# Performance work log

Measured on AMD Instinct MI355X. Metric: run time of the kernel, lower is better.

## Reference

```python
import jax, jax.numpy as jnp
import numpy as np


def setup_inputs() -> dict:
    key = jax.random.key(0)
    k1, k2, k3 = jax.random.split(key, 3)
    B, c_in, T, N = 16, 64, 64, 512
    K, c_out = 3, 64
    x = jax.random.normal(k1, (B, c_in, T, N), dtype=jnp.float32)
    # scaled Laplacian-like matrix; scale to keep Chebyshev recurrence stable
    La = jax.random.normal(k2, (B, N, N), dtype=jnp.float32) / jnp.sqrt(jnp.float32(N))
    # Conv2d(K*c_in, c_out, 1x1, bias=False) weight, squeezed to [c_out, K*c_in]
    W = jax.random.normal(k3, (c_out, K * c_in), dtype=jnp.float32) * 0.05
    return {"x": x, "La": La, "W": W}


def reference(x, La, W):
    # x: [B, c_in, T, N], La: [B, N, N], W: [c_out, K*c_in]
    B, c_in, T, N = x.shape
    K = W.shape[1] // c_in
    xp = jnp.transpose(x, (0, 1, 3, 2))  # [B, c_in, N, T] -> 'bcnl'
    # Chebyshev polynomial recurrence: T0 = I, T1 = La, Tk = 2*La@T_{k-1} - T_{k-2}
    I = jnp.broadcast_to(jnp.eye(N, dtype=x.dtype), (B, N, N))
    Ls = [I, La]
    L0, L1 = I, La
    for _ in range(2, K):
        L2 = 2.0 * jnp.matmul(La, L1) - L0
        L0, L1 = L1, L2
        Ls.append(L2)
    Lap = jnp.stack(Ls, axis=1)            # [B, K, N, N]
    Lap = jnp.swapaxes(Lap, -1, -2)        # transpose(-1,-2) as in torch
    # graph conv: contract over source node n
    y = jnp.einsum('bcnl,bknq->bckql', xp, Lap)  # [B, c_in, K, N, T]
    y = y.reshape(B, c_in * K, N, T)       # channel index = c*K + k
    # 1x1 conv, no bias: [c_out, c_in*K] x [B, c_in*K, N, T]
    out = jnp.einsum('oi,binl->bonl', W, y)  # [B, c_out, N, T]
    out = jnp.transpose(out, (0, 1, 3, 2))   # [B, c_out, T, N]
    return out
```

## Files before the change

### kernel.cpp

```cpp
#include <hip/hip_runtime.h>
#include <hip/hip_bf16.h>


#define B_   16
#define CIN  64
#define T_   64
#define N_   512
#define M_   4096
#define KDIM 512
#define COUT 64

typedef __bf16 bf16x8 __attribute__((ext_vector_type(8)));
typedef float  floatx4 __attribute__((ext_vector_type(4)));

__device__ __forceinline__ float bf2f(unsigned short u) {
    unsigned int v = ((unsigned int)u) << 16;
    return __builtin_bit_cast(float, v);
}
__device__ __forceinline__ unsigned short f2bf(float f) {
    unsigned int u = __builtin_bit_cast(unsigned int, f);
    unsigned int lsb = (u >> 16) & 1u;
    u += 0x7fffu + lsb;
    return (unsigned short)(u >> 16);
}

#define GLOAD_LDS16(gp, lp)                                                  \
    __builtin_amdgcn_global_load_lds(                                        \
        (const __attribute__((address_space(1))) void*)(gp),                 \
        (__attribute__((address_space(3))) void*)(lp), 16, 0, 0)

__global__ __launch_bounds__(256) void cvt_f32_bf16(
    const float* __restrict__ src, unsigned short* __restrict__ dst, int n)
{
    int i = (blockIdx.x * 256 + threadIdx.x) * 8;
    if (i + 8 <= n) {
        float4 a = *(const float4*)(src + i);
        float4 b = *(const float4*)(src + i + 4);
        union { unsigned short s[8]; uint4 u; } o;
        o.s[0] = f2bf(a.x); o.s[1] = f2bf(a.y); o.s[2] = f2bf(a.z); o.s[3] = f2bf(a.w);
        o.s[4] = f2bf(b.x); o.s[5] = f2bf(b.y); o.s[6] = f2bf(b.z); o.s[7] = f2bf(b.w);
        *(uint4*)(dst + i) = o.u;
    }
}

__global__ __launch_bounds__(256) void pack_w(
    const float* __restrict__ W, unsigned short* __restrict__ Wb)
{
    int idx = threadIdx.x + blockIdx.x * 256;
    if (idx < 64 * 192) {
        int o = idx / 192, j = idx % 192;
        int c = j & 63, k = j >> 6;
        Wb[idx] = f2bf(W[o * 192 + c * 3 + k]);
    }
}

#define BM 128
#define BN 128
#define BK 32
#define KIT  (KDIM / BK)
#define SBUF (BM * BK)

__global__ __launch_bounds__(256) void gemm_bt(
    const unsigned short* __restrict__ A,
    const unsigned short* __restrict__ Bm,
    unsigned short* __restrict__ C,
    const unsigned short* __restrict__ X,
    int mode)
{
    int h     = blockIdx.x;
    int g     = h & 7;
    int idx   = h >> 3;
    int batch = g * 2 + (idx >> 7);
    int local = idx & 127;
    int n0    = (local & 3) * BN;
    int m0    = (local >> 2) * BM;

    A  += (size_t)batch * M_ * KDIM;
    Bm += (size_t)batch * N_ * KDIM;
    C  += (size_t)batch * M_ * N_;
    X  += (size_t)batch * M_ * N_;

    __shared__ __align__(16) unsigned short As[3 * SBUF];
    __shared__ __align__(16) unsigned short Bs[3 * SBUF];

    int tid  = threadIdx.x;
    int lane = tid & 63;
    int wave = tid >> 6;
    int wm   = (wave >> 1) * 64;
    int wn   = (wave & 1) * 64;
    int l15  = lane & 15;
    int quad = lane >> 4;

    int r16 = lane >> 2;
    int sch = lane & 3;
    int gch = sch ^ ((r16 >> 1) & 3);

    const unsigned short* gA0 = A  + (size_t)(m0 + wave * 16 + r16) * KDIM + gch * 8;
    const unsigned short* gA1 = gA0 + (size_t)64 * KDIM;
    const unsigned short* gB0 = Bm + (size_t)(n0 + wave * 16 + r16) * KDIM + gch * 8;
    const unsigned short* gB1 = gB0 + (size_t)64 * KDIM;

    int dA0 = (wave * 16) * BK;
    int dA1 = (64 + wave * 16) * BK;
    int dB0 = dA0;
    int dB1 = dA1;

#define STAGE(kk, bo) do {                                        \
        GLOAD_LDS16(gA0 + (kk) * BK, &As[(bo) + dA0]);            \
        GLOAD_LDS16(gA1 + (kk) * BK, &As[(bo) + dA1]);            \
        GLOAD_LDS16(gB0 + (kk) * BK, &Bs[(bo) + dB0]);            \
        GLOAD_LDS16(gB1 + (kk) * BK, &Bs[(bo) + dB1]);            \
    } while (0)

    int aoff[4], boff[4];
    int sl = quad ^ ((l15 >> 1) & 3);
#pragma unroll
    for (int im = 0; im < 4; im++)
        aoff[im] = (wm + im * 16 + l15) * BK + sl * 8;
#pragma unroll
    for (int jn = 0; jn < 4; jn++)
        boff[jn] = (wn + jn * 16 + l15) * BK + sl * 8;

    floatx4 acc[4][4];
#pragma unroll
    for (int i = 0; i < 4; i++)
#pragma unroll
        for (int j = 0; j < 4; j++) acc[i][j] = (floatx4)0.0f;

    STAGE(0, 0);
    STAGE(1, SBUF);

#pragma unroll
    for (int k = 0; k < KIT; ++k) {
        if (k < KIT - 1) asm volatile("s_waitcnt vmcnt(4)" ::: "memory");
        else             asm volatile("s_waitcnt vmcnt(0)" ::: "memory");
        __builtin_amdgcn_s_barrier();

        if (k + 2 < KIT) STAGE(k + 2, ((k + 2) % 3) * SBUF);

        const int cb = (k % 3) * SBUF;
        bf16x8 af[4], bf[4];
#pragma unroll
        for (int im = 0; im < 4; im++)
            af[im] = __builtin_bit_cast(bf16x8, *(const uint4*)&As[cb + aoff[im]]);
#pragma unroll
        for (int jn = 0; jn < 4; jn++)
            bf[jn] = __builtin_bit_cast(bf16x8, *(const uint4*)&Bs[cb + boff[jn]]);
#pragma unroll
        for (int im = 0; im < 4; im++)
#pragma unroll
            for (int jn = 0; jn < 4; jn++)
                acc[im][jn] = __builtin_amdgcn_mfma_f32_16x16x32_bf16(
                    af[im], bf[jn], acc[im][jn], 0, 0, 0);
    }
#undef STAGE

#pragma unroll
    for (int im = 0; im < 4; im++)
#pragma unroll
        for (int jn = 0; jn < 4; jn++) {
            int c = n0 + wn + jn * 16 + l15;
#pragma unroll
            for (int r = 0; r < 4; r++) {
                int m = m0 + wm + im * 16 + quad * 4 + r;
                size_t idx2 = (size_t)m * N_ + c;
                float v = acc[im][jn][r];
                if (mode) v = 2.0f * v - bf2f(X[idx2]);
                C[idx2] = f2bf(v);
            }
        }
}

#define PJ_PITCH 40

__global__ __launch_bounds__(256) void proj(
    const unsigned short* __restrict__ xb,
    const unsigned short* __restrict__ z1b,
    const unsigned short* __restrict__ z2b,
    const unsigned short* __restrict__ Wb,
    float* __restrict__ out)
{
    __shared__ __align__(16) unsigned short Ds[256 * PJ_PITCH];

    int b  = blockIdx.y;
    int n0 = blockIdx.x * 256;
    int tid  = threadIdx.x;
    int lane = tid & 63;
    int wave = tid >> 6;
    int l15  = lane & 15;
    int quad = lane >> 4;

    size_t boff = (size_t)b * M_ * N_ + n0;
    const unsigned short* zp[3] = { xb + boff, z1b + boff, z2b + boff };

    bf16x8 wf[6];
#pragma unroll
    for (int kc = 0; kc < 6; kc++)
        wf[kc] = __builtin_bit_cast(bf16x8,
            *(const uint4*)(Wb + (size_t)(wave * 16 + l15) * 192 + kc * 32 + quad * 8));

    floatx4 acc[16];
#pragma unroll
    for (int i = 0; i < 16; i++) acc[i] = (floatx4)0.0f;

    int jl  = tid & 31;
    int nc0 = (tid >> 5) * 8;

    for (int kc = 0; kc < 6; kc++) {
        const unsigned short* src =
            zp[kc >> 1] + (size_t)((kc & 1) * 32 + jl) * (T_ * N_) + nc0;
        uint4 v[4];
#pragma unroll
        for (int u = 0; u < 4; u++) v[u] = *(const uint4*)(src + u * 64);

        __syncthreads();
#pragma unroll
        for (int u = 0; u < 4; u++) {
            unsigned short* d = &Ds[(size_t)(nc0 + u * 64) * PJ_PITCH + jl];
            unsigned int w0 = v[u].x, w1 = v[u].y, w2 = v[u].z, w3 = v[u].w;
            d[0 * PJ_PITCH] = (unsigned short)w0;
            d[1 * PJ_PITCH] = (unsigned short)(w0 >> 16);
            d[2 * PJ_PITCH] = (unsigned short)w1;
            d[3 * PJ_PITCH] = (unsigned short)(w1 >> 16);
            d[4 * PJ_PITCH] = (unsigned short)w2;
            d[5 * PJ_PITCH] = (unsigned short)(w2 >> 16);
            d[6 * PJ_PITCH] = (unsigned short)w3;
            d[7 * PJ_PITCH] = (unsigned short)(w3 >> 16);
        }
        __syncthreads();

#pragma unroll
        for (int nt = 0; nt < 16; nt++) {
            bf16x8 bfr = __builtin_bit_cast(bf16x8,
                *(const uint4*)(&Ds[(size_t)(nt * 16 + l15) * PJ_PITCH + quad * 8]));
            acc[nt] = __builtin_amdgcn_mfma_f32_16x16x32_bf16(wf[kc], bfr, acc[nt], 0, 0, 0);
        }
    }

    float* ob = out + (size_t)b * COUT * (T_ * N_);
#pragma unroll
    for (int nt = 0; nt < 16; nt++) {
        int n = n0 + nt * 16 + l15;
#pragma unroll
        for (int r = 0; r < 4; r++) {
            int o = wave * 16 + quad * 4 + r;
            ob[(size_t)o * (T_ * N_) + n] = acc[nt][r];
        }
    }
}

extern "C" void kernel_launch(void* const* d_in, const int* in_sizes, int n_in,
                              void* d_out, int out_size, void* d_ws, size_t ws_size,
                              hipStream_t stream) {
    const float* x  = (const float*)d_in[0];
    const float* La = (const float*)d_in[1];
    const float* W  = (const float*)d_in[2];
    float* out = (float*)d_out;

    const size_t n_x  = (size_t)B_ * CIN * T_ * N_;
    const size_t n_La = (size_t)B_ * N_ * N_;

    char* ws = (char*)d_ws;
    unsigned short* xb  = (unsigned short*)ws;
    unsigned short* Lab = (unsigned short*)(ws + n_x * 2);
    unsigned short* z1b = (unsigned short*)(ws + n_x * 2 + n_La * 2);
    unsigned short* z2b = (unsigned short*)(ws + n_x * 4 + n_La * 2);
    unsigned short* Wb  = (unsigned short*)(ws + n_x * 6 + n_La * 2);

    cvt_f32_bf16<<<(int)(n_x / 2048),  256, 0, stream>>>(x,  xb,  (int)n_x);
    cvt_f32_bf16<<<(int)(n_La / 2048), 256, 0, stream>>>(La, Lab, (int)n_La);
    pack_w<<<48, 256, 0, stream>>>(W, Wb);

    gemm_bt<<<2048, 256, 0, stream>>>(xb,  Lab, z1b, xb, 0);
    gemm_bt<<<2048, 256, 0, stream>>>(z1b, Lab, z2b, xb, 1);

    dim3 gp((T_ * N_) / 256, B_);
    proj<<<gp, 256, 0, stream>>>(xb, z1b, z2b, Wb, out);
}
```

Baseline: 424.7 us.

## Precompute La squared and fuse both Chebyshev GEMMs into one pass over x

Builds a transposed bf16 copy of La during conversion, computes La·La per batch with a small GEMM, then runs one fused GEMM that reads the x tile once and multiplies it against both La and La², writing z1 and z2 = 2·x·La² − x. This removes the dependent second large GEMM and its re-read of z1, at the cost of an extra small N×N GEMM, more shared memory (three staging buffers) and twice the accumulator registers per thread. Rounding La² to bf16 before use also changes numerics slightly.

```diff
diff --git a/kernel.cpp b/kernel.cpp
--- a/kernel.cpp
+++ b/kernel.cpp
@@ -43,6 +43,46 @@
     }
 }
 
+__global__ __launch_bounds__(256) void cvt_la_dual(
+    const float* __restrict__ La,
+    unsigned short* __restrict__ Lab,
+    unsigned short* __restrict__ LaT)
+{
+    __shared__ unsigned short t64[64][68];
+    int b  = blockIdx.z;
+    int r0 = blockIdx.y * 64;
+    int c0 = blockIdx.x * 64;
+    int t   = threadIdx.x;
+    int row = t >> 2;
+    int cg  = (t & 3) * 16;
+
+    const float* src = La + (size_t)b * N_ * N_ + (size_t)(r0 + row) * N_ + c0 + cg;
+    unsigned short s[16];
+#pragma unroll
+    for (int u = 0; u < 4; u++) {
+        float4 f = *(const float4*)(src + u * 4);
+        s[u * 4 + 0] = f2bf(f.x); s[u * 4 + 1] = f2bf(f.y);
+        s[u * 4 + 2] = f2bf(f.z); s[u * 4 + 3] = f2bf(f.w);
+    }
+    union { unsigned short h[8]; uint4 u; } p0, p1;
+#pragma unroll
+    for (int u = 0; u < 8; u++) { p0.h[u] = s[u]; p1.h[u] = s[8 + u]; }
+    unsigned short* d0 = Lab + (size_t)b * N_ * N_ + (size_t)(r0 + row) * N_ + c0 + cg;
+    *(uint4*)d0 = p0.u;
+    *(uint4*)(d0 + 8) = p1.u;
+#pragma unroll
+    for (int u = 0; u < 16; u++) t64[row][cg + u] = s[u];
+    __syncthreads();
+    int col = t >> 2;
+    int rg  = (t & 3) * 16;
+    union { unsigned short h[8]; uint4 u; } q0, q1;
+#pragma unroll
+    for (int u = 0; u < 8; u++) { q0.h[u] = t64[rg + u][col]; q1.h[u] = t64[rg + 8 + u][col]; }
+    unsigned short* d1 = LaT + (size_t)b * N_ * N_ + (size_t)(c0 + col) * N_ + r0 + rg;
+    *(uint4*)d1 = q0.u;
+    *(uint4*)(d1 + 8) = q1.u;
+}
+
 __global__ __launch_bounds__(256) void pack_w(
     const float* __restrict__ W, unsigned short* __restrict__ Wb)
 {
@@ -60,12 +100,112 @@
 #define KIT  (KDIM / BK)
 #define SBUF (BM * BK)
 
-__global__ __launch_bounds__(256) void gemm_bt(
+__global__ __launch_bounds__(256) void gemm_la2(
     const unsigned short* __restrict__ A,
     const unsigned short* __restrict__ Bm,
-    unsigned short* __restrict__ C,
-    const unsigned short* __restrict__ X,
-    int mode)
+    unsigned short* __restrict__ C)
+{
+    int h     = blockIdx.x;
+    int g     = h & 7;
+    int idx   = h >> 3;
+    int batch = g * 2 + (idx >> 4);
+    int local = idx & 15;
+    int n0    = (local & 3) * BN;
+    int m0    = (local >> 2) * BM;
+
+    A  += (size_t)batch * N_ * KDIM;
+    Bm += (size_t)batch * N_ * KDIM;
+    C  += (size_t)batch * N_ * N_;
+
+    __shared__ __align__(16) unsigned short As[3 * SBUF];
+    __shared__ __align__(16) unsigned short Bs[3 * SBUF];
+
+    int tid  = threadIdx.x;
+    int lane = tid & 63;
+    int wave = tid >> 6;
+    int wm   = (wave >> 1) * 64;
+    int wn   = (wave & 1) * 64;
+    int l15  = lane & 15;
+    int quad = lane >> 4;
+
+    int r16 = lane >> 2;
+    int sch = lane & 3;
+    int gch = sch ^ ((r16 >> 1) & 3);
+
+    const unsigned short* gA0 = A  + (size_t)(m0 + wave * 16 + r16) * KDIM + gch * 8;
+    const unsigned short* gA1 = gA0 + (size_t)64 * KDIM;
+    const unsigned short* gB0 = Bm + (size_t)(n0 + wave * 16 + r16) * KDIM + gch * 8;
+    const unsigned short* gB1 = gB0 + (size_t)64 * KDIM;
+
+    int dA0 = (wave * 16) * BK;
+    int dA1 = (64 + wave * 16) * BK;
+
+#define STAGE2(kk, bo) do {                                       \
+        GLOAD_LDS16(gA0 + (kk) * BK, &As[(bo) + dA0]);            \
+        GLOAD_LDS16(gA1 + (kk) * BK, &As[(bo) + dA1]);            \
+        GLOAD_LDS16(gB0 + (kk) * BK, &Bs[(bo) + dA0]);            \
+        GLOAD_LDS16(gB1 + (kk) * BK, &Bs[(bo) + dA1]);            \
+    } while (0)
+
+    int aoff[4], boff[4];
+    int sl = quad ^ ((l15 >> 1) & 3);
+#pragma unroll
+    for (int im = 0; im < 4; im++) aoff[im] = (wm + im * 16 + l15) * BK + sl * 8;
+#pragma unroll
+    for (int jn = 0; jn < 4; jn++) boff[jn] = (wn + jn * 16 + l15) * BK + sl * 8;
+
+    floatx4 acc[4][4];
+#pragma unroll
+    for (int i = 0; i < 4; i++)
+#pragma unroll
+        for (int j = 0; j < 4; j++) acc[i][j] = (floatx4)0.0f;
+
+    STAGE2(0, 0);
+    STAGE2(1, SBUF);
+
+#pragma unroll
+    for (int k = 0; k < KIT; ++k) {
+        if (k < KIT - 1) asm volatile("s_waitcnt vmcnt(4)" ::: "memory");
+        else             asm volatile("s_waitcnt vmcnt(0)" ::: "memory");
+        __builtin_amdgcn_s_barrier();
+        if (k + 2 < KIT) STAGE2(k + 2, ((k + 2) % 3) * SBUF);
+
+        const int cb = (k % 3) * SBUF;
+        bf16x8 af[4], bf[4];
+#pragma unroll
+        for (int im = 0; im < 4; im++)
+            af[im] = __builtin_bit_cast(bf16x8, *(const uint4*)&As[cb + aoff[im]]);
+#pragma unroll
+        for (int jn = 0; jn < 4; jn++)
+            bf[jn] = __builtin_bit_cast(bf16x8, *(const uint4*)&Bs[cb + boff[jn]]);
+#pragma unroll
+        for (int im = 0; im < 4; im++)
+#pragma unroll
+            for (int jn = 0; jn < 4; jn++)
+                acc[im][jn] = __builtin_amdgcn_mfma_f32_16x16x32_bf16(
+                    af[im], bf[jn], acc[im][jn], 0, 0, 0);
+    }
+#undef STAGE2
+
+#pragma unroll
+    for (int im = 0; im < 4; im++)
+#pragma unroll
+        for (int jn = 0; jn < 4; jn++) {
+            int c = n0 + wn + jn * 16 + l15;
+#pragma unroll
+            for (int r = 0; r < 4; r++) {
+                int m = m0 + wm + im * 16 + quad * 4 + r;
+                C[(size_t)m * N_ + c] = f2bf(acc[im][jn][r]);
+            }
+        }
+}
+
+__global__ __launch_bounds__(256) void gemm_fused(
+    const unsigned short* __restrict__ A,
+    const unsigned short* __restrict__ B1,
+    const unsigned short* __restrict__ B2,
+    unsigned short* __restrict__ Z1,
+    unsigned short* __restrict__ Z2)
 {
     int h     = blockIdx.x;
     int g     = h & 7;
@@ -76,12 +216,14 @@
     int m0    = (local >> 2) * BM;
 
     A  += (size_t)batch * M_ * KDIM;
-    Bm += (size_t)batch * N_ * KDIM;
-    C  += (size_t)batch * M_ * N_;
-    X  += (size_t)batch * M_ * N_;
-
-    __shared__ __align__(16) unsigned short As[3 * SBUF];
-    __shared__ __align__(16) unsigned short Bs[3 * SBUF];
+    B1 += (size_t)batch * N_ * KDIM;
+    B2 += (size_t)batch * N_ * KDIM;
+    Z1 += (size_t)batch * M_ * N_;
+    Z2 += (size_t)batch * M_ * N_;
+
+    __shared__ __align__(16) unsigned short As [3 * SBUF];
+    __shared__ __align__(16) unsigned short Bs1[3 * SBUF];
+    __shared__ __align__(16) unsigned short Bs2[3 * SBUF];
 
     int tid  = threadIdx.x;
     int lane = tid & 63;
@@ -95,66 +237,71 @@
     int sch = lane & 3;
     int gch = sch ^ ((r16 >> 1) & 3);
 
-    const unsigned short* gA0 = A  + (size_t)(m0 + wave * 16 + r16) * KDIM + gch * 8;
-    const unsigned short* gA1 = gA0 + (size_t)64 * KDIM;
-    const unsigned short* gB0 = Bm + (size_t)(n0 + wave * 16 + r16) * KDIM + gch * 8;
-    const unsigned short* gB1 = gB0 + (size_t)64 * KDIM;
-
-    int dA0 = (wave * 16) * BK;
-    int dA1 = (64 + wave * 16) * BK;
-    int dB0 = dA0;
-    int dB1 = dA1;
-
-#define STAGE(kk, bo) do {                                        \
-        GLOAD_LDS16(gA0 + (kk) * BK, &As[(bo) + dA0]);            \
-        GLOAD_LDS16(gA1 + (kk) * BK, &As[(bo) + dA1]);            \
-        GLOAD_LDS16(gB0 + (kk) * BK, &Bs[(bo) + dB0]);            \
-        GLOAD_LDS16(gB1 + (kk) * BK, &Bs[(bo) + dB1]);            \
+    const unsigned short* gA0  = A  + (size_t)(m0 + wave * 16 + r16) * KDIM + gch * 8;
+    const unsigned short* gA1  = gA0 + (size_t)64 * KDIM;
+    const unsigned short* gB10 = B1 + (size_t)(n0 + wave * 16 + r16) * KDIM + gch * 8;
+    const unsigned short* gB11 = gB10 + (size_t)64 * KDIM;
+    const unsigned short* gB20 = B2 + (size_t)(n0 + wave * 16 + r16) * KDIM + gch * 8;
+    const unsigned short* gB21 = gB20 + (size_t)64 * KDIM;
+
+    int d0 = (wave * 16) * BK;
+    int d1 = (64 + wave * 16) * BK;
+
+#define STAGE6(kk, bo) do {                                        \
+        GLOAD_LDS16(gA0  + (kk) * BK, &As [(bo) + d0]);            \
+        GLOAD_LDS16(gA1  + (kk) * BK, &As [(bo) + d1]);            \
+        GLOAD_LDS16(gB10 + (kk) * BK, &Bs1[(bo) + d0]);            \
+        GLOAD_LDS16(gB11 + (kk) * BK, &Bs1[(bo) + d1]);            \
+        GLOAD_LDS16(gB20 + (kk) * BK, &Bs2[(bo) + d0]);            \
+        GLOAD_LDS16(gB21 + (kk) * BK, &Bs2[(bo) + d1]);            \
     } while (0)
 
     int aoff[4], boff[4];
     int sl = quad ^ ((l15 >> 1) & 3);
 #pragma unroll
-    for (int im = 0; im < 4; im++)
-        aoff[im] = (wm + im * 16 + l15) * BK + sl * 8;
-#pragma unroll
-    for (int jn = 0; jn < 4; jn++)
-        boff[jn] = (wn + jn * 16 + l15) * BK + sl * 8;
-
-    floatx4 acc[4][4];
+    for (int im = 0; im < 4; im++) aoff[im] = (wm + im * 16 + l15) * BK + sl * 8;
+#pragma unroll
+    for (int jn = 0; jn < 4; jn++) boff[jn] = (wn + jn * 16 + l15) * BK + sl * 8;
+
+    floatx4 acc1[4][4], acc2[4][4];
 #pragma unroll
     for (int i = 0; i < 4; i++)
 #pragma unroll
-        for (int j = 0; j < 4; j++) acc[i][j] = (floatx4)0.0f;
-
-    STAGE(0, 0);
-    STAGE(1, SBUF);
+        for (int j = 0; j < 4; j++) { acc1[i][j] = (floatx4)0.0f; acc2[i][j] = (floatx4)0.0f; }
+
+    STAGE6(0, 0);
+    STAGE6(1, SBUF);
 
 #pragma unroll
     for (int k = 0; k < KIT; ++k) {
-        if (k < KIT - 1) asm volatile("s_waitcnt vmcnt(4)" ::: "memory");
+        if (k < KIT - 1) asm volatile("s_waitcnt vmcnt(6)" ::: "memory");
         else             asm volatile("s_waitcnt vmcnt(0)" ::: "memory");
         __builtin_amdgcn_s_barrier();
-
-        if (k + 2 < KIT) STAGE(k + 2, ((k + 2) % 3) * SBUF);
+        if (k + 2 < KIT) STAGE6(k + 2, ((k + 2) % 3) * SBUF);
 
         const int cb = (k % 3) * SBUF;
-        bf16x8 af[4], bf[4];
+        bf16x8 af[4], bf1[4], bf2[4];
 #pragma unroll
         for (int im = 0; im < 4; im++)
             af[im] = __builtin_bit_cast(bf16x8, *(const uint4*)&As[cb + aoff[im]]);
 #pragma unroll
-        for (int jn = 0; jn < 4; jn++)
-            bf[jn] = __builtin_bit_cast(bf16x8, *(const uint4*)&Bs[cb + boff[jn]]);
+        for (int jn = 0; jn < 4; jn++) {
+            bf1[jn] = __builtin_bit_cast(bf16x8, *(const uint4*)&Bs1[cb + boff[jn]]);
+            bf2[jn] = __builtin_bit_cast(bf16x8, *(const uint4*)&Bs2[cb + boff[jn]]);
+        }
 #pragma unroll
         for (int im = 0; im < 4; im++)
 #pragma unroll
-            for (int jn = 0; jn < 4; jn++)
-                acc[im][jn] = __builtin_amdgcn_mfma_f32_16x16x32_bf16(
-                    af[im], bf[jn], acc[im][jn], 0, 0, 0);
-    }
-#undef STAGE
-
+            for (int jn = 0; jn < 4; jn++) {
+                acc1[im][jn] = __builtin_amdgcn_mfma_f32_16x16x32_bf16(
+                    af[im], bf1[jn], acc1[im][jn], 0, 0, 0);
+                acc2[im][jn] = __builtin_amdgcn_mfma_f32_16x16x32_bf16(
+                    af[im], bf2[jn], acc2[im][jn], 0, 0, 0);
+            }
+    }
+#undef STAGE6
+
+    const unsigned short* Xb = A;
 #pragma unroll
     for (int im = 0; im < 4; im++)
 #pragma unroll
@@ -164,9 +311,8 @@
             for (int r = 0; r < 4; r++) {
                 int m = m0 + wm + im * 16 + quad * 4 + r;
                 size_t idx2 = (size_t)m * N_ + c;
-                float v = acc[im][jn][r];
-                if (mode) v = 2.0f * v - bf2f(X[idx2]);
-                C[idx2] = f2bf(v);
+                Z1[idx2] = f2bf(acc1[im][jn][r]);
+                Z2[idx2] = f2bf(2.0f * acc2[im][jn][r] - bf2f(Xb[idx2]));
             }
         }
 }
@@ -261,18 +407,21 @@
     const size_t n_La = (size_t)B_ * N_ * N_;
 
     char* ws = (char*)d_ws;
-    unsigned short* xb  = (unsigned short*)ws;
-    unsigned short* Lab = (unsigned short*)(ws + n_x * 2);
-    unsigned short* z1b = (unsigned short*)(ws + n_x * 2 + n_La * 2);
-    unsigned short* z2b = (unsigned short*)(ws + n_x * 4 + n_La * 2);
-    unsigned short* Wb  = (unsigned short*)(ws + n_x * 6 + n_La * 2);
-
-    cvt_f32_bf16<<<(int)(n_x / 2048),  256, 0, stream>>>(x,  xb,  (int)n_x);
-    cvt_f32_bf16<<<(int)(n_La / 2048), 256, 0, stream>>>(La, Lab, (int)n_La);
+    unsigned short* xb   = (unsigned short*)ws;
+    unsigned short* Lab  = (unsigned short*)(ws + n_x * 2);
+    unsigned short* z1b  = (unsigned short*)(ws + n_x * 2 + n_La * 2);
+    unsigned short* z2b  = (unsigned short*)(ws + n_x * 4 + n_La * 2);
+    unsigned short* Wb   = (unsigned short*)(ws + n_x * 6 + n_La * 2);
+    unsigned short* LaT  = (unsigned short*)(ws + n_x * 6 + n_La * 2 + (1 << 20));
+    unsigned short* La2b = (unsigned short*)(ws + n_x * 6 + n_La * 4 + (1 << 20));
+
+    cvt_f32_bf16<<<(int)(n_x / 2048), 256, 0, stream>>>(x, xb, (int)n_x);
+    cvt_la_dual<<<dim3(8, 8, 16), 256, 0, stream>>>(La, Lab, LaT);
     pack_w<<<48, 256, 0, stream>>>(W, Wb);
 
-    gemm_bt<<<2048, 256, 0, stream>>>(xb,  Lab, z1b, xb, 0);
-    gemm_bt<<<2048, 256, 0, stream>>>(z1b, Lab, z2b, xb, 1);
+    gemm_la2<<<256, 256, 0, stream>>>(Lab, LaT, La2b);
+
+    gemm_fused<<<2048, 256, 0, stream>>>(xb, Lab, La2b, z1b, z2b);
 
     dim3 gp((T_ * N_) / 256, B_);
     proj<<<gp, 256, 0, stream>>>(xb, z1b, z2b, Wb, out);
```

Measured after the change: 438.1 us. +3.2%, slower.
